# Kernel tuning notes

Hardware: AMD Instinct MI355X
Metric: run time of the kernel (lower is better)

Reference implementation:

```python
import jax, jax.numpy as jnp
import numpy as np

FEATURES = 256
HIDDEN = 256
NUM_BINS = 10
NUM_BLOCKS = 2
MULT = 2 * NUM_BINS + 1  # tails=None -> widths(K) + heights(K+1)
MIN_BW = 1e-3
MIN_BH = 1e-3
BATCH = 8192


def _build_masks():
    # nflows MADE sequential degrees
    in_deg = np.arange(1, FEATURES + 1)
    hid_deg = np.arange(HIDDEN) % max(1, FEATURES - 1) + min(1, FEATURES - 1)
    m0 = (hid_deg[:, None] >= in_deg[None, :]).astype(np.float32)   # [H, F]
    mh = (hid_deg[:, None] >= hid_deg[None, :]).astype(np.float32)  # [H, H]
    out_deg = np.repeat(in_deg, MULT)                               # feature-major tiling (nflows _tile)
    mf = (out_deg[:, None] > hid_deg[None, :]).astype(np.float32)   # [F*MULT, H]
    return jnp.asarray(m0), jnp.asarray(mh), jnp.asarray(mf)

MASK0, MASKH, MASKF = _build_masks()


def setup_inputs() -> dict:
    key = jax.random.key(0)
    ks = jax.random.split(key, 7)
    s = 1.0 / np.sqrt(HIDDEN)
    return {
        "inputs": jax.random.uniform(ks[0], (BATCH, FEATURES), dtype=jnp.float32),
        "W0": jax.random.normal(ks[1], (HIDDEN, FEATURES), dtype=jnp.float32) * s,
        "b0": jax.random.normal(ks[2], (HIDDEN,), dtype=jnp.float32) * 0.01,
        "Wb": jax.random.normal(ks[3], (2 * NUM_BLOCKS, HIDDEN, HIDDEN), dtype=jnp.float32) * s,
        "bb": jax.random.normal(ks[4], (2 * NUM_BLOCKS, HIDDEN), dtype=jnp.float32) * 0.01,
        "Wf": jax.random.normal(ks[5], (FEATURES * MULT, HIDDEN), dtype=jnp.float32) * s,
        "bf": jax.random.normal(ks[6], (FEATURES * MULT,), dtype=jnp.float32) * 0.01,
    }


def _made(x, W0, b0, Wb, bb, Wf, bf):
    h = x @ (W0 * MASK0).T + b0
    for i in range(NUM_BLOCKS):  # pre-activation masked residual blocks
        t = jax.nn.relu(h)
        t = t @ (Wb[2 * i] * MASKH).T + bb[2 * i]
        t = jax.nn.relu(t)
        t = t @ (Wb[2 * i + 1] * MASKH).T + bb[2 * i + 1]
        h = h + t
    return h @ (Wf * MASKF).T + bf  # [B, F*MULT]


def _quadratic_spline(x, uw, uh):
    # x: [B,F]; uw: [B,F,K]; uh: [B,F,K+1]
    widths = jax.nn.softmax(uw, axis=-1)
    widths = MIN_BW + (1.0 - MIN_BW * NUM_BINS) * widths
    hexp = jnp.exp(uh)
    area = jnp.sum(0.5 * (hexp[..., :-1] + hexp[..., 1:]) * widths, axis=-1, keepdims=True)
    heights = hexp / area
    heights = MIN_BH + (1.0 - MIN_BH) * heights

    cdf = jnp.cumsum(0.5 * (heights[..., :-1] + heights[..., 1:]) * widths, axis=-1)
    cdf = cdf.at[..., -1].set(1.0)
    cdf = jnp.pad(cdf, [(0, 0), (0, 0), (1, 0)])
    locs = jnp.cumsum(widths, axis=-1)
    locs = locs.at[..., -1].set(1.0)
    locs = jnp.pad(locs, [(0, 0), (0, 0), (1, 0)])

    # searchsorted: sum(x >= knots) - 1, clamped into valid bins
    idx = jnp.clip(jnp.sum(x[..., None] >= locs, axis=-1) - 1, 0, NUM_BINS - 1)
    g = lambda t, i: jnp.take_along_axis(t, i[..., None], axis=-1)[..., 0]

    loc = g(locs, idx)
    w = g(widths, idx)
    lcdf = g(cdf, idx)
    hl = g(heights, idx)
    hr = g(heights, idx + 1)

    a = 0.5 * (hr - hl) * w
    b = hl * w
    alpha = (x - loc) / w
    out = jnp.clip(a * alpha * alpha + b * alpha + lcdf, 0.0, 1.0)
    logabsdet = jnp.log(alpha * (hr - hl) + hl)
    return out, jnp.sum(logabsdet, axis=-1)  # sum_except_batch


def reference(inputs, W0, b0, Wb, bb, Wf, bf):
    params = _made(inputs, W0, b0, Wb, bb, Wf, bf)
    tp = params.reshape(inputs.shape[0], FEATURES, MULT)
    scale = 1.0 / np.sqrt(HIDDEN).astype(np.float32)
    uw = tp[..., :NUM_BINS] * scale
    uh = tp[..., NUM_BINS:] * scale
    return _quadratic_spline(inputs, uw, uh)
```

## Files before the change

kernel.cpp:

```cpp
#include <hip/hip_runtime.h>

typedef _Float16 f16;
typedef f16 f16x8 __attribute__((ext_vector_type(8)));
typedef float f32x4 __attribute__((ext_vector_type(4)));

#define MFMA(A,B,C) __builtin_amdgcn_mfma_f32_16x16x32_f16(A,B,C,0,0,0)

#define PTRUNK 0u
#define PHEAD  655360u

__device__ __forceinline__ void fsplit(float v, f16& hi, f16& lo) {
    hi = (f16)v;
    lo = (f16)(v - (float)hi);
}

__global__ __launch_bounds__(256) void prep_kernel(
    const float* __restrict__ W0, const float* __restrict__ Wb,
    const float* __restrict__ Wf, unsigned char* __restrict__ wsb)
{
    const int id   = blockIdx.x * 256 + threadIdx.x;
    const int lane = id & 63;
    const int frag = id >> 6;
    const int li = lane & 15, lg = lane >> 4;
    if (frag < 640) {
        int ct = frag & 15, ks = (frag >> 4) & 7, mat = frag >> 7;
        int c  = ct * 16 + li;
        int k0 = ks * 32 + lg * 8;
        const float* src = (mat == 0) ? (W0 + c * 256)
                                      : (Wb + (mat - 1) * 65536 + c * 256);
        int cd = c % 255;
        f16 v[8];
        #pragma unroll
        for (int e = 0; e < 8; ++e) {
            int k = k0 + e;
            bool act = (mat == 0) ? (cd >= k) : (cd >= (k % 255));
            v[e] = act ? (f16)src[k] : (f16)0.f;
        }
        ((f16x8*)(wsb + PTRUNK))[frag * 64 + lane] = *(f16x8*)v;
    } else {
        int hfrag = frag - 640;
        int ct  = hfrag % 21;
        int tmp = hfrag / 21;
        int ks  = tmp & 7;
        int bly = tmp >> 3;
        int cl  = ct * 16 + li;
        int f   = bly * 16 + cl / 21;
        int m   = cl % 21;
        int k0  = ks * 32 + lg * 8;
        f16 v[8];
        #pragma unroll
        for (int e = 0; e < 8; ++e) {
            int k = k0 + e;
            int j = (k == 0) ? 255 : (k - 1);
            int jd = j % 255;
            float wv = (f > jd) ? Wf[(f * 21 + m) * 256 + j] : 0.f;
            v[e] = (f16)wv;
        }
        ((f16x8*)(wsb + PHEAD))[hfrag * 64 + lane] = *(f16x8*)v;
    }
}

__global__ __launch_bounds__(256, 2) void mega_kernel(
    const float* __restrict__ x, const unsigned char* __restrict__ wsb,
    const float* __restrict__ b0, const float* __restrict__ bb,
    const float* __restrict__ bfp, float* __restrict__ out,
    float* __restrict__ lad)
{
    __shared__ f16  Ah[2][16][280];
    __shared__ f16  Al[2][16][280];
    __shared__ float prm[4][16][100];
    __shared__ float ladp[4][16];

    const int t = threadIdx.x, lane = t & 63;
    const int wu = __builtin_amdgcn_readfirstlane(t >> 6);
    const int li = lane & 15, lg = lane >> 4;
    const int r0 = blockIdx.x * 16;

    {
        int row = t >> 4, cb = (t & 15) * 16;
        const float* xr = x + (r0 + row) * 256 + cb;
        f16 hi[16], lo[16];
        #pragma unroll
        for (int j = 0; j < 16; j += 4) {
            float4 v4 = *(const float4*)(xr + j);
            fsplit(v4.x, hi[j],     lo[j]);
            fsplit(v4.y, hi[j + 1], lo[j + 1]);
            fsplit(v4.z, hi[j + 2], lo[j + 2]);
            fsplit(v4.w, hi[j + 3], lo[j + 3]);
        }
        *(f16x8*)&Ah[0][row][cb]     = *(f16x8*)&hi[0];
        *(f16x8*)&Ah[0][row][cb + 8] = *(f16x8*)&hi[8];
        *(f16x8*)&Al[0][row][cb]     = *(f16x8*)&lo[0];
        *(f16x8*)&Al[0][row][cb + 8] = *(f16x8*)&lo[8];
    }
    __syncthreads();

    const f16x8* wt = (const f16x8*)(wsb + PTRUNK);
    const f16x8* wh = (const f16x8*)(wsb + PHEAD);

    f32x4 h[4], acc[4];
    const int nkp = 2 * wu + 2;

    auto gemm = [&](int mat, int src, int add7, const float* __restrict__ bias) {
        #pragma unroll
        for (int ci = 0; ci < 4; ++ci) acc[ci] = (f32x4){0.f, 0.f, 0.f, 0.f};
        #pragma unroll
        for (int ks = 0; ks < 8; ++ks) {
            if (ks < nkp || (add7 && ks == 7)) {
                f16x8 ah = *(const f16x8*)&Ah[src][li][ks * 32 + lg * 8];
                f16x8 al = *(const f16x8*)&Al[src][li][ks * 32 + lg * 8];
                #pragma unroll
                for (int ci = 0; ci < 4; ++ci) {
                    f16x8 bv = wt[mat * 8192 + (ks * 16 + wu * 4 + ci) * 64 + lane];
                    acc[ci] = MFMA(al, bv, acc[ci]);
                    acc[ci] = MFMA(ah, bv, acc[ci]);
                }
            }
        }
        #pragma unroll
        for (int ci = 0; ci < 4; ++ci) {
            float bv = bias[(wu * 4 + ci) * 16 + li];
            #pragma unroll
            for (int q = 0; q < 4; ++q) acc[ci][q] += bv;
        }
    };

    auto store_act = [&](int dst, f32x4* s, bool relu, bool rot) {
        #pragma unroll
        for (int ci = 0; ci < 4; ++ci) {
            int c  = (wu * 4 + ci) * 16 + li;
            int cc = rot ? ((c + 1) & 255) : c;
            #pragma unroll
            for (int q = 0; q < 4; ++q) {
                float v = s[ci][q];
                if (relu) v = fmaxf(v, 0.f);
                f16 hi, lo; fsplit(v, hi, lo);
                Ah[dst][lg * 4 + q][cc] = hi;
                Al[dst][lg * 4 + q][cc] = lo;
            }
        }
    };

    gemm(0, 0, 0, b0);
    #pragma unroll
    for (int ci = 0; ci < 4; ++ci) h[ci] = acc[ci];
    store_act(1, acc, true, false);
    __syncthreads();

    gemm(1, 1, (wu < 3) ? 1 : 0, bb + 0);
    store_act(0, acc, true, false);
    __syncthreads();

    gemm(2, 0, (wu < 3) ? 1 : 0, bb + 256);
    #pragma unroll
    for (int ci = 0; ci < 4; ++ci) h[ci] += acc[ci];
    store_act(1, h, true, false);
    __syncthreads();

    gemm(3, 1, (wu < 3) ? 1 : 0, bb + 512);
    store_act(0, acc, true, false);
    __syncthreads();

    gemm(4, 0, (wu < 3) ? 1 : 0, bb + 768);
    #pragma unroll
    for (int ci = 0; ci < 4; ++ci) h[ci] += acc[ci];
    store_act(1, h, false, true);
    __syncthreads();

    float ladreg = 0.f;

    for (int ib = 0; ib < 4; ++ib) {
        const int bly = ib * 4 + wu;
        const int nloop = (bly + 2) >> 1;
        const int f0 = bly * 16;

        #pragma unroll
        for (int pass = 0; pass < 4; ++pass) {
            const int f = f0 + pass * 4 + lg;
            const float xv = x[(r0 + li) * 256 + f];

            f32x4 hacc[6];
            #pragma unroll
            for (int ci = 0; ci < 6; ++ci) hacc[ci] = (f32x4){0.f, 0.f, 0.f, 0.f};

            #pragma unroll
            for (int s = 0; s < 8; ++s) {
                if (s < nloop) {
                    f16x8 ah = *(const f16x8*)&Ah[1][li][s * 32 + lg * 8];
                    f16x8 al = *(const f16x8*)&Al[1][li][s * 32 + lg * 8];
                    #pragma unroll
                    for (int ci = 0; ci < 6; ++ci) {
                        f16x8 bv = wh[((bly * 8 + s) * 21 + pass * 5 + ci) * 64 + lane];
                        hacc[ci] = MFMA(al, bv, hacc[ci]);
                        hacc[ci] = MFMA(ah, bv, hacc[ci]);
                    }
                }
            }

            asm volatile("s_waitcnt lgkmcnt(0)" ::: "memory");

            #pragma unroll
            for (int ci = 0; ci < 6; ++ci) {
                int cl = (pass * 5 + ci) * 16 + li;
                int fw = cl / 21;
                int m  = cl - fw * 21;
                if (fw >= pass * 4 && fw < pass * 4 + 4) {
                    float bv = bfp[f0 * 21 + cl];
                    #pragma unroll
                    for (int q = 0; q < 4; ++q)
                        prm[wu][lg * 4 + q][(fw - pass * 4) * 24 + m] =
                            (hacc[ci][q] + bv) * 0.0625f;
                }
            }
            asm volatile("s_waitcnt lgkmcnt(0)" ::: "memory");

            float p[21];
            #pragma unroll
            for (int m = 0; m < 21; ++m) p[m] = prm[wu][li][lg * 24 + m];

            float wmax = p[0];
            #pragma unroll
            for (int i = 1; i < 10; ++i) wmax = fmaxf(wmax, p[i]);
            float ew[10]; float wsum = 0.f;
            #pragma unroll
            for (int i = 0; i < 10; ++i) { ew[i] = __expf(p[i] - wmax); wsum += ew[i]; }
            float winv = 1.0f / wsum;
            float wid[10];
            #pragma unroll
            for (int i = 0; i < 10; ++i) wid[i] = 1.0e-3f + 0.99f * ew[i] * winv;

            float hx[11];
            #pragma unroll
            for (int i = 0; i < 11; ++i) hx[i] = __expf(p[10 + i]);
            float area = 0.f;
            #pragma unroll
            for (int i = 0; i < 10; ++i) area += 0.5f * (hx[i] + hx[i + 1]) * wid[i];
            float ainv = 1.0f / area;
            float hts[11];
            #pragma unroll
            for (int i = 0; i < 11; ++i) hts[i] = 1.0e-3f + 0.999f * hx[i] * ainv;

            float cdf[11], locs[11];
            cdf[0] = 0.f; locs[0] = 0.f;
            float ca = 0.f, la = 0.f;
            #pragma unroll
            for (int i = 0; i < 10; ++i) {
                ca += 0.5f * (hts[i] + hts[i + 1]) * wid[i];
                la += wid[i];
                cdf[i + 1] = ca; locs[i + 1] = la;
            }
            cdf[10] = 1.0f; locs[10] = 1.0f;

            int cntk = 0;
            #pragma unroll
            for (int i = 0; i < 11; ++i) cntk += (xv >= locs[i]) ? 1 : 0;
            int idx = cntk - 1;
            idx = idx < 0 ? 0 : (idx > 9 ? 9 : idx);

            float loc = 0.f, ww = 0.f, lc = 0.f, hl = 0.f, hr = 0.f;
            #pragma unroll
            for (int i = 0; i < 10; ++i)
                if (i == idx) { loc = locs[i]; ww = wid[i]; lc = cdf[i]; hl = hts[i]; hr = hts[i + 1]; }

            float aq  = 0.5f * (hr - hl) * ww;
            float bq2 = hl * ww;
            float al2 = (xv - loc) / ww;
            float y = (aq * al2 + bq2) * al2 + lc;
            y = fminf(fmaxf(y, 0.f), 1.f);
            out[(r0 + li) * 256 + f] = y;

            ladreg += __logf(al2 * (hr - hl) + hl);
        }
    }

    ladreg += __shfl_xor(ladreg, 16);
    ladreg += __shfl_xor(ladreg, 32);
    if (lane < 16) ladp[wu][lane] = ladreg;
    __syncthreads();
    if (t < 16)
        lad[r0 + t] = ladp[0][t] + ladp[1][t] + ladp[2][t] + ladp[3][t];
}

extern "C" void kernel_launch(void* const* d_in, const int* in_sizes, int n_in,
                              void* d_out, int out_size, void* d_ws, size_t ws_size,
                              hipStream_t stream)
{
    const float* x  = (const float*)d_in[0];
    const float* W0 = (const float*)d_in[1];
    const float* b0 = (const float*)d_in[2];
    const float* Wb = (const float*)d_in[3];
    const float* bb = (const float*)d_in[4];
    const float* Wf = (const float*)d_in[5];
    const float* bf = (const float*)d_in[6];

    float* out = (float*)d_out;
    float* lad = out + 8192 * 256;
    unsigned char* wsb = (unsigned char*)d_ws;

    prep_kernel<<<832, 256, 0, stream>>>(W0, Wb, Wf, wsb);
    mega_kernel<<<512, 256, 0, stream>>>(x, wsb, b0, bb, bf, out, lad);
}
```

Measured before the change: 162.2 us.

## Double-buffer weight fragment loads in GEMMs and coalesce prep via LDS transpose

The trunk and head GEMM loops now use runtime-length loops with two register buffers (bA/bB), so global weight-fragment loads for the next k-step are issued before the MFMAs of the current step. The prep kernel now reads weight rows with float4 loads, stages them in shared memory and writes the fragment layout from there, which halves its block count and replaces strided scalar reads. The explicit lgkmcnt waits around the prm shared-memory exchange are removed. The double buffering raises register pressure in a kernel with launch bounds (256,2). Dropping the waits relies on the compiler to order the LDS write and read correctly.

```diff
diff --git a/kernel.cpp b/kernel.cpp
--- a/kernel.cpp
+++ b/kernel.cpp
@@ -18,45 +18,65 @@
     const float* __restrict__ W0, const float* __restrict__ Wb,
     const float* __restrict__ Wf, unsigned char* __restrict__ wsb)
 {
-    const int id   = blockIdx.x * 256 + threadIdx.x;
-    const int lane = id & 63;
-    const int frag = id >> 6;
-    const int li = lane & 15, lg = lane >> 4;
-    if (frag < 640) {
-        int ct = frag & 15, ks = (frag >> 4) & 7, mat = frag >> 7;
-        int c  = ct * 16 + li;
-        int k0 = ks * 32 + lg * 8;
-        const float* src = (mat == 0) ? (W0 + c * 256)
-                                      : (Wb + (mat - 1) * 65536 + c * 256);
-        int cd = c % 255;
-        f16 v[8];
-        #pragma unroll
-        for (int e = 0; e < 8; ++e) {
-            int k = k0 + e;
-            bool act = (mat == 0) ? (cd >= k) : (cd >= (k % 255));
-            v[e] = act ? (f16)src[k] : (f16)0.f;
-        }
-        ((f16x8*)(wsb + PTRUNK))[frag * 64 + lane] = *(f16x8*)v;
+    __shared__ f16 sm[16][264];
+    const int b = blockIdx.x, t = threadIdx.x;
+    const int cr = t >> 4, kc = t & 15;
+
+    if (b < 80) {
+        const int mat = b >> 4, ct = b & 15;
+        const int c = ct * 16 + cr;
+        const int cd = c % 255;
+        const float* src = ((mat == 0) ? W0 : (Wb + (mat - 1) * 65536)) + c * 256;
+        #pragma unroll
+        for (int u = 0; u < 4; ++u) {
+            const int k = kc * 16 + u * 4;
+            float4 v = *(const float4*)(src + k);
+            float vv[4] = {v.x, v.y, v.z, v.w};
+            #pragma unroll
+            for (int e = 0; e < 4; ++e) {
+                int kk = k + e;
+                int kd = (mat == 0) ? kk : (kk % 255);
+                sm[cr][kk] = (cd >= kd) ? (f16)vv[e] : (f16)0.f;
+            }
+        }
+        __syncthreads();
+        const int ks = t >> 5, ln = t & 31;
+        #pragma unroll
+        for (int rep = 0; rep < 2; ++rep) {
+            const int L = ln + rep * 32;
+            const int li = L & 15, lg = L >> 4;
+            f16x8 v = *(const f16x8*)&sm[li][ks * 32 + lg * 8];
+            ((f16x8*)(wsb + PTRUNK))[(mat * 128 + ks * 16 + ct) * 64 + L] = v;
+        }
     } else {
-        int hfrag = frag - 640;
-        int ct  = hfrag % 21;
-        int tmp = hfrag / 21;
-        int ks  = tmp & 7;
-        int bly = tmp >> 3;
-        int cl  = ct * 16 + li;
-        int f   = bly * 16 + cl / 21;
-        int m   = cl % 21;
-        int k0  = ks * 32 + lg * 8;
-        f16 v[8];
-        #pragma unroll
-        for (int e = 0; e < 8; ++e) {
-            int k = k0 + e;
-            int j = (k == 0) ? 255 : (k - 1);
-            int jd = j % 255;
-            float wv = (f > jd) ? Wf[(f * 21 + m) * 256 + j] : 0.f;
-            v[e] = (f16)wv;
-        }
-        ((f16x8*)(wsb + PHEAD))[hfrag * 64 + lane] = *(f16x8*)v;
+        const int hb = b - 80;
+        const int bly = hb / 21, ct = hb - bly * 21;
+        const int cl = ct * 16 + cr;
+        const int fw = cl / 21;
+        const int f  = bly * 16 + fw;
+        const int m  = cl - fw * 21;
+        const float* src = Wf + (f * 21 + m) * 256;
+        #pragma unroll
+        for (int u = 0; u < 4; ++u) {
+            const int k = kc * 16 + u * 4;
+            float4 v = *(const float4*)(src + k);
+            float vv[4] = {v.x, v.y, v.z, v.w};
+            #pragma unroll
+            for (int e = 0; e < 4; ++e) {
+                int kk = k + e;
+                int jd = kk % 255;
+                sm[cr][(kk + 1) & 255] = (f > jd) ? (f16)vv[e] : (f16)0.f;
+            }
+        }
+        __syncthreads();
+        const int ks = t >> 5, ln = t & 31;
+        #pragma unroll
+        for (int rep = 0; rep < 2; ++rep) {
+            const int L = ln + rep * 32;
+            const int li = L & 15, lg = L >> 4;
+            f16x8 v = *(const f16x8*)&sm[li][ks * 32 + lg * 8];
+            ((f16x8*)(wsb + PHEAD))[((bly * 8 + ks) * 21 + ct) * 64 + L] = v;
+        }
     }
 }
 
@@ -104,16 +124,37 @@
     auto gemm = [&](int mat, int src, int add7, const float* __restrict__ bias) {
         #pragma unroll
         for (int ci = 0; ci < 4; ++ci) acc[ci] = (f32x4){0.f, 0.f, 0.f, 0.f};
-        #pragma unroll
-        for (int ks = 0; ks < 8; ++ks) {
-            if (ks < nkp || (add7 && ks == 7)) {
+        const int tot = nkp + add7;
+        const f16x8* wb = wt + mat * 8192;
+        f16x8 bA[4], bB[4];
+        #pragma unroll
+        for (int ci = 0; ci < 4; ++ci) bA[ci] = wb[(wu * 4 + ci) * 64 + lane];
+        for (int s = 0; s < tot; s += 2) {
+            const int ks1 = (s + 1 < nkp) ? (s + 1) : 7;
+            #pragma unroll
+            for (int ci = 0; ci < 4; ++ci)
+                bB[ci] = wb[(ks1 * 16 + wu * 4 + ci) * 64 + lane];
+            {
+                const int ks = (s < nkp) ? s : 7;
                 f16x8 ah = *(const f16x8*)&Ah[src][li][ks * 32 + lg * 8];
                 f16x8 al = *(const f16x8*)&Al[src][li][ks * 32 + lg * 8];
                 #pragma unroll
                 for (int ci = 0; ci < 4; ++ci) {
-                    f16x8 bv = wt[mat * 8192 + (ks * 16 + wu * 4 + ci) * 64 + lane];
-                    acc[ci] = MFMA(al, bv, acc[ci]);
-                    acc[ci] = MFMA(ah, bv, acc[ci]);
+                    acc[ci] = MFMA(al, bA[ci], acc[ci]);
+                    acc[ci] = MFMA(ah, bA[ci], acc[ci]);
+                }
+            }
+            const int ks2 = (s + 2 < nkp) ? (s + 2) : 7;
+            #pragma unroll
+            for (int ci = 0; ci < 4; ++ci)
+                bA[ci] = wb[(ks2 * 16 + wu * 4 + ci) * 64 + lane];
+            if (s + 1 < tot) {
+                f16x8 ah = *(const f16x8*)&Ah[src][li][ks1 * 32 + lg * 8];
+                f16x8 al = *(const f16x8*)&Al[src][li][ks1 * 32 + lg * 8];
+                #pragma unroll
+                for (int ci = 0; ci < 4; ++ci) {
+                    acc[ci] = MFMA(al, bB[ci], acc[ci]);
+                    acc[ci] = MFMA(ah, bB[ci], acc[ci]);
                 }
             }
         }
@@ -171,7 +212,7 @@
 
     for (int ib = 0; ib < 4; ++ib) {
         const int bly = ib * 4 + wu;
-        const int nloop = (bly + 2) >> 1;
+        const int nl = (bly + 2) >> 1;
         const int f0 = bly * 16;
 
         #pragma unroll
@@ -183,21 +224,39 @@
             #pragma unroll
             for (int ci = 0; ci < 6; ++ci) hacc[ci] = (f32x4){0.f, 0.f, 0.f, 0.f};
 
-            #pragma unroll
-            for (int s = 0; s < 8; ++s) {
-                if (s < nloop) {
+            f16x8 bA[6], bB[6];
+            #pragma unroll
+            for (int ci = 0; ci < 6; ++ci)
+                bA[ci] = wh[((bly * 8) * 21 + pass * 5 + ci) * 64 + lane];
+
+            for (int s = 0; s < nl; s += 2) {
+                const int s1 = (s + 1 < nl) ? (s + 1) : (nl - 1);
+                #pragma unroll
+                for (int ci = 0; ci < 6; ++ci)
+                    bB[ci] = wh[((bly * 8 + s1) * 21 + pass * 5 + ci) * 64 + lane];
+                {
                     f16x8 ah = *(const f16x8*)&Ah[1][li][s * 32 + lg * 8];
                     f16x8 al = *(const f16x8*)&Al[1][li][s * 32 + lg * 8];
                     #pragma unroll
                     for (int ci = 0; ci < 6; ++ci) {
-                        f16x8 bv = wh[((bly * 8 + s) * 21 + pass * 5 + ci) * 64 + lane];
-                        hacc[ci] = MFMA(al, bv, hacc[ci]);
-                        hacc[ci] = MFMA(ah, bv, hacc[ci]);
+                        hacc[ci] = MFMA(al, bA[ci], hacc[ci]);
+                        hacc[ci] = MFMA(ah, bA[ci], hacc[ci]);
                     }
                 }
-            }
-
-            asm volatile("s_waitcnt lgkmcnt(0)" ::: "memory");
+                const int s2 = (s + 2 < nl) ? (s + 2) : (nl - 1);
+                #pragma unroll
+                for (int ci = 0; ci < 6; ++ci)
+                    bA[ci] = wh[((bly * 8 + s2) * 21 + pass * 5 + ci) * 64 + lane];
+                if (s + 1 < nl) {
+                    f16x8 ah = *(const f16x8*)&Ah[1][li][s1 * 32 + lg * 8];
+                    f16x8 al = *(const f16x8*)&Al[1][li][s1 * 32 + lg * 8];
+                    #pragma unroll
+                    for (int ci = 0; ci < 6; ++ci) {
+                        hacc[ci] = MFMA(al, bB[ci], hacc[ci]);
+                        hacc[ci] = MFMA(ah, bB[ci], hacc[ci]);
+                    }
+                }
+            }
 
             #pragma unroll
             for (int ci = 0; ci < 6; ++ci) {
@@ -212,7 +271,6 @@
                             (hacc[ci][q] + bv) * 0.0625f;
                 }
             }
-            asm volatile("s_waitcnt lgkmcnt(0)" ::: "memory");
 
             float p[21];
             #pragma unroll
@@ -297,6 +355,6 @@
     float* lad = out + 8192 * 256;
     unsigned char* wsb = (unsigned char*)d_ws;
 
-    prep_kernel<<<832, 256, 0, stream>>>(W0, Wb, Wf, wsb);
+    prep_kernel<<<416, 256, 0, stream>>>(W0, Wb, Wf, wsb);
     mega_kernel<<<512, 256, 0, stream>>>(x, wsb, b0, bb, bf, out, lad);
 }
```

Result: faster. 149.6 us (-7.8%).
